# Optimization experiments

Measured on AMD Instinct MI355X. Metric: run time of the kernel, lower is better.

## Reference

```python
import jax, jax.numpy as jnp
import numpy as np
from jax import tree_util as jtu

B, N, DIM = 2, 2048, 512
HEADS, DH = 4, 128
CHUNK = 64
NC = N // CHUNK
DHID = 4 * DH  # expansion_factor 4
MAX_LR = 1.0   # default_step_transform_max_lr


def rms_norm(x, g, eps=1e-6):
    var = jnp.mean(jnp.square(x), axis=-1, keepdims=True)
    return x * jax.lax.rsqrt(var + eps) * g


def mem_model(params, x):
    # ResidualNorm(MemoryMLP depth=2): out = mlp(rmsnorm(x)) + x
    g, w1, w2 = params
    h = rms_norm(x, g)
    h = jax.nn.gelu(jnp.dot(h, w1), approximate=False)
    h = jnp.dot(h, w2)
    return h + x


def _expand(a, leaf):
    # broadcast a per-(b*h) scalar gate over a weight leaf
    return a.reshape(a.shape + (1,) * (leaf.ndim - 1))


def neural_memory(seq, g_store, g_retrieve, Wq, Wk, Wv, Wa, ba, Wm, Wd, bd, Wg, Wc, mem_g, w1, w2):
    xs = rms_norm(seq, g_store)      # store_norm
    xr = rms_norm(seq, g_retrieve)   # retrieve_norm

    def split_heads(t):
        return t.reshape(B, N, HEADS, DH).transpose(0, 2, 1, 3)  # b h n d

    k = split_heads(xs @ Wk)
    v = split_heads(xs @ Wv)
    q = split_heads(xr @ Wq)

    # adaptive per-token lr (sigmoid * max_lr)
    lr = (jax.nn.sigmoid(xs @ Wa + ba) * MAX_LR).transpose(0, 2, 1)  # [B,H,N]
    # per-chunk pooled stats drive momentum + decay gates (AveragePool)
    pooled = xs.reshape(B, NC, CHUNK, DIM).mean(axis=2)              # [B,NC,DIM]
    beta = jax.nn.sigmoid(pooled @ Wm)                               # momentum factor [B,NC,H]
    alpha = 1.0 - jax.nn.sigmoid(pooled @ Wd + bd)                   # weight-retain (1-decay)

    BH = B * HEADS
    k_c = k.reshape(BH, NC, CHUNK, DH)
    v_c = v.reshape(BH, NC, CHUNK, DH)
    q_c = q.reshape(BH, NC, CHUNK, DH)
    lr_c = lr.reshape(BH, NC, CHUNK)
    beta_t = beta.transpose(0, 2, 1).reshape(BH, NC).T   # [NC,BH]
    alpha_t = alpha.transpose(0, 2, 1).reshape(BH, NC).T

    # per-head memory params repeated over batch*heads (per_head_learned_parameters)
    init_params = (
        jnp.broadcast_to(mem_g, (B, HEADS, DH)).reshape(BH, DH),
        jnp.broadcast_to(w1, (B, HEADS, DH, DHID)).reshape(BH, DH, DHID),
        jnp.broadcast_to(w2, (B, HEADS, DHID, DH)).reshape(BH, DHID, DH),
    )

    def chunk_loss(params, kc, vc, lrc):
        pred = mem_model(params, kc)                              # [CHUNK,DH]
        return jnp.sum(jnp.mean(jnp.square(pred - vc), axis=-1) * lrc)

    # per-chunk 'surprise' gradients: vmap over (b*h) and chunks, grads wrt init weights
    grad_fn = jax.grad(chunk_loss)
    grads = jax.vmap(jax.vmap(grad_fn, in_axes=(None, 0, 0, 0)), in_axes=(0, 0, 0, 0))(
        init_params, k_c, v_c, lr_c)
    sur_t = jtu.tree_map(lambda g: jnp.moveaxis(-g, 1, 0), grads)  # [NC,BH,...]

    # momentum recurrence: m_t = beta_t * m_{t-1} + surprise_t
    def mom_step(m, inp):
        b, s = inp
        m = jtu.tree_map(lambda mm, ss: _expand(b, mm) * mm + ss, m, s)
        return m, m
    m0 = jtu.tree_map(lambda t: jnp.zeros_like(t[0]), sur_t)
    _, upd_t = jax.lax.scan(mom_step, m0, (beta_t, sur_t))

    # weight recurrence with decay: w_t = (1-decay_t) * w_{t-1} + m_t
    def w_step(w, inp):
        a, u = inp
        w = jtu.tree_map(lambda ww, uu: _expand(a, ww) * ww + uu, w, u)
        return w, w
    _, w_t = jax.lax.scan(w_step, init_params, (alpha_t, upd_t))

    # causal retrieval: chunk i reads weights updated through chunk i-1
    w_prev = jtu.tree_map(
        lambda wt, w0: jnp.moveaxis(jnp.concatenate([w0[None], wt[:-1]], axis=0), 0, 1),
        w_t, init_params)                                          # [BH,NC,...]

    retrieved = jax.vmap(jax.vmap(mem_model))(w_prev, q_c)         # [BH,NC,CHUNK,DH]
    retrieved = retrieved.reshape(B, HEADS, N, DH)
    gate = jax.nn.sigmoid(xr @ Wg).transpose(0, 2, 1)[..., None]   # retrieve_gate [B,H,N,1]
    retrieved = retrieved * gate
    out = retrieved.transpose(0, 2, 1, 3).reshape(B, N, HEADS * DH) @ Wc  # combine_heads
    return out


def setup_inputs():
    key = jax.random.key(0)
    ks = jax.random.split(key, 12)
    s = 0.02
    f = jnp.float32
    return {
        "seq": jax.random.normal(ks[0], (B, N, DIM), f),
        "g_store": jnp.ones((DIM,), f),
        "g_retrieve": jnp.ones((DIM,), f),
        "Wq": jax.random.normal(ks[1], (DIM, HEADS * DH), f) * s,
        "Wk": jax.random.normal(ks[2], (DIM, HEADS * DH), f) * s,
        "Wv": jax.random.normal(ks[3], (DIM, HEADS * DH), f) * s,
        "Wa": jax.random.normal(ks[4], (DIM, HEADS), f) * s,
        "ba": jnp.zeros((HEADS,), f),
        "Wm": jax.random.normal(ks[5], (DIM, HEADS), f) * s,
        "Wd": jax.random.normal(ks[6], (DIM, HEADS), f) * s,
        "bd": jnp.zeros((HEADS,), f),
        "Wg": jax.random.normal(ks[7], (DIM, HEADS), f) * s,
        "Wc": jax.random.normal(ks[8], (HEADS * DH, DIM), f) * s,
        "mem_g": jnp.ones((DH,), f),
        "w1": jax.random.normal(ks[9], (DH, DHID), f) * (1.0 / np.sqrt(DH)),
        "w2": jax.random.normal(ks[10], (DHID, DH), f) * (1.0 / np.sqrt(DHID)),
    }


def reference(seq, g_store, g_retrieve, Wq, Wk, Wv, Wa, ba, Wm, Wd, bd, Wg, Wc, mem_g, w1, w2):
    return neural_memory(seq, g_store, g_retrieve, Wq, Wk, Wv, Wa, ba, Wm, Wd, bd, Wg, Wc, mem_g, w1, w2)
```

## Files before the change

kernel.cpp:

```cpp
#include <hip/hip_runtime.h>
#include <hip/hip_bf16.h>

#define B_ 2
#define N_ 2048
#define DIM_ 512
#define H_ 4
#define DH_ 128
#define DHID_ 512
#define CH_ 64
#define NC_ 32
#define BH_ 8

typedef __bf16 bf16x8 __attribute__((ext_vector_type(8)));
typedef float f32x4 __attribute__((ext_vector_type(4)));

__device__ __forceinline__ f32x4 MFMA(bf16x8 a, bf16x8 b, f32x4 c) {
    return __builtin_amdgcn_mfma_f32_16x16x32_bf16(a, b, c, 0, 0, 0);
}
__device__ __forceinline__ bf16x8 ld8(const __bf16* p) { return *(const bf16x8*)p; }

__device__ __forceinline__ float sigmoidf_(float x) { return 1.0f / (1.0f + expf(-x)); }
__device__ __forceinline__ float gelu_f(float x) {
    return x * 0.5f * (1.0f + erff(x * 0.7071067811865476f));
}
__device__ __forceinline__ float gelu_g(float x) {
    float cdf = 0.5f * (1.0f + erff(x * 0.7071067811865476f));
    float pdf = 0.3989422804014327f * expf(-0.5f * x * x);
    return cdf + x * pdf;
}

__global__ __launch_bounds__(256) void rms_kernel(
    const float* __restrict__ seq, const float* __restrict__ gs,
    const float* __restrict__ gr, const float* __restrict__ Wa,
    const float* __restrict__ ba, const float* __restrict__ Wg,
    float* __restrict__ xs, float* __restrict__ xr,
    __bf16* __restrict__ xsb, __bf16* __restrict__ xrb,
    float* __restrict__ lrb, float* __restrict__ gateb)
{
    const int row = blockIdx.x;
    const int t = threadIdx.x;
    const int wave = t >> 6, lane = t & 63;
    const float* x = seq + (size_t)row * DIM_;
    float v0 = x[t], v1 = x[t + 256];
    float ss = v0 * v0 + v1 * v1;
#pragma unroll
    for (int off = 32; off; off >>= 1) ss += __shfl_xor(ss, off);
    __shared__ float red[4];
    __shared__ float red2[4][8];
    if (lane == 0) red[wave] = ss;
    __syncthreads();
    float tot = red[0] + red[1] + red[2] + red[3];
    float r = rsqrtf(tot * (1.0f / DIM_) + 1e-6f);
    size_t o = (size_t)row * DIM_;
    float a0 = v0 * r * gs[t], a1 = v1 * r * gs[t + 256];
    float b0 = v0 * r * gr[t], b1 = v1 * r * gr[t + 256];
    xs[o + t] = a0; xs[o + t + 256] = a1;
    xr[o + t] = b0; xr[o + t + 256] = b1;
    xsb[o + t] = (__bf16)a0; xsb[o + t + 256] = (__bf16)a1;
    xrb[o + t] = (__bf16)b0; xrb[o + t + 256] = (__bf16)b1;
    float pa[4], pg[4];
#pragma unroll
    for (int h = 0; h < 4; ++h) {
        pa[h] = a0 * Wa[t * 4 + h] + a1 * Wa[(t + 256) * 4 + h];
        pg[h] = b0 * Wg[t * 4 + h] + b1 * Wg[(t + 256) * 4 + h];
    }
#pragma unroll
    for (int h = 0; h < 4; ++h)
#pragma unroll
        for (int off = 32; off; off >>= 1) {
            pa[h] += __shfl_xor(pa[h], off);
            pg[h] += __shfl_xor(pg[h], off);
        }
    if (lane == 0) {
#pragma unroll
        for (int h = 0; h < 4; ++h) {
            red2[wave][h] = pa[h];
            red2[wave][4 + h] = pg[h];
        }
    }
    __syncthreads();
    if (t < 8) {
        float s = red2[0][t] + red2[1][t] + red2[2][t] + red2[3][t];
        int b = row >> 11, n = row & 2047;
        if (t < 4) lrb[(size_t)(b * 4 + t) * N_ + n] = sigmoidf_(s + ba[t]);
        else gateb[(size_t)(b * 4 + (t - 4)) * N_ + n] = sigmoidf_(s);
    }
}

__global__ __launch_bounds__(256) void ba_kernel(
    const float* __restrict__ xs, const float* __restrict__ Wm,
    const float* __restrict__ Wd, const float* __restrict__ bd,
    float* __restrict__ beta, float* __restrict__ alpha)
{
    const int b = blockIdx.x >> 5, ci = blockIdx.x & 31;
    const int t = threadIdx.x;
    const int wave = t >> 6, lane = t & 63;
    const float* base = xs + ((size_t)b * N_ + ci * CH_) * DIM_;
    const int d0 = t * 2;
    float s0 = 0.f, s1 = 0.f;
#pragma unroll 8
    for (int r = 0; r < CH_; ++r) {
        s0 += base[(size_t)r * DIM_ + d0];
        s1 += base[(size_t)r * DIM_ + d0 + 1];
    }
    s0 *= (1.0f / CH_); s1 *= (1.0f / CH_);
    float pm[4], pd[4];
#pragma unroll
    for (int h = 0; h < 4; ++h) {
        pm[h] = s0 * Wm[d0 * 4 + h] + s1 * Wm[(d0 + 1) * 4 + h];
        pd[h] = s0 * Wd[d0 * 4 + h] + s1 * Wd[(d0 + 1) * 4 + h];
    }
#pragma unroll
    for (int h = 0; h < 4; ++h)
#pragma unroll
        for (int off = 32; off; off >>= 1) {
            pm[h] += __shfl_xor(pm[h], off);
            pd[h] += __shfl_xor(pd[h], off);
        }
    __shared__ float red2[4][8];
    if (lane == 0) {
#pragma unroll
        for (int h = 0; h < 4; ++h) {
            red2[wave][h] = pm[h];
            red2[wave][4 + h] = pd[h];
        }
    }
    __syncthreads();
    if (t < 4) {
        float sm = red2[0][t] + red2[1][t] + red2[2][t] + red2[3][t];
        float sd = red2[0][4 + t] + red2[1][4 + t] + red2[2][4 + t] + red2[3][4 + t];
        int bh = b * 4 + t;
        beta[bh * NC_ + ci] = sigmoidf_(sm);
        alpha[bh * NC_ + ci] = 1.0f - sigmoidf_(sd + bd[t]);
    }
}

__global__ __launch_bounds__(256) void prep_kernel(
    const float* __restrict__ w1, const float* __restrict__ w2,
    const float* __restrict__ Wq, const float* __restrict__ Wk,
    const float* __restrict__ Wv, const float* __restrict__ Wc,
    __bf16* __restrict__ w1b, __bf16* __restrict__ w1Tb,
    __bf16* __restrict__ w2b, __bf16* __restrict__ w2Tb,
    __bf16* __restrict__ WqT, __bf16* __restrict__ WkT,
    __bf16* __restrict__ WvT, __bf16* __restrict__ WcT)
{
    int idx = blockIdx.x * 256 + threadIdx.x;
    if (idx < 65536) {
        w1b[idx] = (__bf16)w1[idx];
        int j = idx >> 7, d = idx & 127;
        w1Tb[idx] = (__bf16)w1[(size_t)d * DHID_ + j];
        w2b[idx] = (__bf16)w2[idx];
        int d2 = idx >> 9, j2 = idx & 511;
        w2Tb[idx] = (__bf16)w2[(size_t)j2 * DH_ + d2];
    }
    int n = idx >> 9, k = idx & 511;
    WqT[idx] = (__bf16)Wq[(size_t)k * 512 + n];
    WkT[idx] = (__bf16)Wk[(size_t)k * 512 + n];
    WvT[idx] = (__bf16)Wv[(size_t)k * 512 + n];
    WcT[idx] = (__bf16)Wc[(size_t)k * 512 + n];
}

__global__ __launch_bounds__(256, 4) void proj_kernel(
    const __bf16* __restrict__ xsb, const __bf16* __restrict__ xrb,
    const __bf16* __restrict__ WqT, const __bf16* __restrict__ WkT,
    const __bf16* __restrict__ WvT,
    float* __restrict__ qb, float* __restrict__ kb, float* __restrict__ vb)
{
    const int z = blockIdx.z;
    const __bf16* A = (z == 0) ? xrb : xsb;
    const __bf16* WT = (z == 0) ? WqT : (z == 1 ? WkT : WvT);
    float* out = (z == 0) ? qb : (z == 1 ? kb : vb);
    const int t = threadIdx.x;
    const int wave = t >> 6, lane = t & 63;
    const int lrow = lane & 15, lgrp = lane >> 4;
    const int c0 = blockIdx.x * 64 + wave * 16;
    const int col0 = blockIdx.y * 64;
    f32x4 acc[4];
#pragma unroll
    for (int i = 0; i < 4; ++i) acc[i] = (f32x4)0.f;
    const __bf16* ar = A + (size_t)(c0 + lrow) * 512;
#pragma unroll 4
    for (int k0 = 0; k0 < 512; k0 += 32) {
        bf16x8 av = ld8(ar + k0 + lgrp * 8);
#pragma unroll
        for (int ct = 0; ct < 4; ++ct) {
            bf16x8 bv = ld8(WT + (size_t)(col0 + ct * 16 + lrow) * 512 + k0 + lgrp * 8);
            acc[ct] = MFMA(av, bv, acc[ct]);
        }
    }
#pragma unroll
    for (int ct = 0; ct < 4; ++ct)
#pragma unroll
        for (int r = 0; r < 4; ++r) {
            int row = c0 + lgrp * 4 + r, col = col0 + ct * 16 + lrow;
            int b = row >> 11, n = row & 2047, h = col >> 7, d = col & 127;
            out[((((size_t)(b * H_ + h) * NC_ + (n >> 6)) * CH_) + (n & 63)) * DH_ + d] = acc[ct][r];
        }
}

__global__ __launch_bounds__(256, 4) void gemm_out(
    const __bf16* __restrict__ A, const __bf16* __restrict__ WT, float* __restrict__ out)
{
    const int t = threadIdx.x;
    const int wave = t >> 6, lane = t & 63;
    const int lrow = lane & 15, lgrp = lane >> 4;
    const int c0 = blockIdx.x * 64 + wave * 16;
    const int col0 = blockIdx.y * 64;
    f32x4 acc[4];
#pragma unroll
    for (int i = 0; i < 4; ++i) acc[i] = (f32x4)0.f;
    const __bf16* ar = A + (size_t)(c0 + lrow) * 512;
#pragma unroll 4
    for (int k0 = 0; k0 < 512; k0 += 32) {
        bf16x8 av = ld8(ar + k0 + lgrp * 8);
#pragma unroll
        for (int ct = 0; ct < 4; ++ct) {
            bf16x8 bv = ld8(WT + (size_t)(col0 + ct * 16 + lrow) * 512 + k0 + lgrp * 8);
            acc[ct] = MFMA(av, bv, acc[ct]);
        }
    }
#pragma unroll
    for (int ct = 0; ct < 4; ++ct)
#pragma unroll
        for (int r = 0; r < 4; ++r) {
            int row = c0 + lgrp * 4 + r, col = col0 + ct * 16 + lrow;
            out[(size_t)row * 512 + col] = acc[ct][r];
        }
}

__global__ __launch_bounds__(1024) void grad_kernel(
    const float* __restrict__ kbuf, const float* __restrict__ vbuf,
    const float* __restrict__ lrbuf, const float* __restrict__ memg,
    const __bf16* __restrict__ w1b, const __bf16* __restrict__ w1Tb,
    const __bf16* __restrict__ w2b, const __bf16* __restrict__ w2Tb,
    float* __restrict__ sg, __bf16* __restrict__ sw1, __bf16* __restrict__ sw2)
{
    const int blk = blockIdx.x;
    const int t = threadIdx.x;
    const int w = t >> 6, lane = t & 63;
    const int lrow = lane & 15, lgrp = lane >> 4;
    const int bh = blk >> 5, nc = blk & 31;
    const float* kc = kbuf + (size_t)blk * (CH_ * DH_);
    const float* vc = vbuf + (size_t)blk * (CH_ * DH_);
    const float* lrp = lrbuf + (size_t)bh * N_ + nc * CH_;
    __bf16* sw1_blk = sw1 + (size_t)blk * (DHID_ * DH_);
    __bf16* sw2_blk = sw2 + (size_t)blk * (DHID_ * DH_);

    __shared__ __bf16 h_s[64][136];
    __shared__ __bf16 e_s[64][136];
    __shared__ __bf16 a_s[64][136];
    __shared__ __bf16 dz_s[64][136];
    __shared__ __bf16 hT_s[128][72];
    __shared__ __bf16 eT_s[128][72];
    __shared__ __bf16 aT_s[128][72];
    __shared__ __bf16 dzT_s[128][72];
    __shared__ float r_s[64];
    __shared__ float lr_s[64];
    __shared__ float g_s[128];
    __shared__ float part_s[2][128];

    if (t < 128) g_s[t] = memg[t];
    if (t < 64) lr_s[t] = lrp[t];
    {
        const int c = t >> 4, i8 = t & 15, d0 = i8 * 8;
        float xv[8];
        float ss = 0.f;
#pragma unroll
        for (int i = 0; i < 2; ++i) {
            float4 f = *(const float4*)(kc + (size_t)c * DH_ + d0 + i * 4);
            xv[i * 4 + 0] = f.x; xv[i * 4 + 1] = f.y; xv[i * 4 + 2] = f.z; xv[i * 4 + 3] = f.w;
            ss += f.x * f.x + f.y * f.y + f.z * f.z + f.w * f.w;
        }
        ss += __shfl_xor(ss, 1); ss += __shfl_xor(ss, 2);
        ss += __shfl_xor(ss, 4); ss += __shfl_xor(ss, 8);
        float r = rsqrtf(ss * (1.0f / DH_) + 1e-6f);
        if (i8 == 0) r_s[c] = r;
        __syncthreads();
#pragma unroll
        for (int i = 0; i < 8; ++i)
            h_s[c][d0 + i] = (__bf16)(xv[i] * r * g_s[d0 + i]);
    }
    __syncthreads();
    {
        const int d = t >> 3, c0 = (t & 7) * 8;
#pragma unroll
        for (int i = 0; i < 8; ++i) hT_s[d][c0 + i] = h_s[c0 + i][d];
    }
    __syncthreads();

    const int cs = w & 3, dq = w >> 2;
    const int c0w = cs * 16, q0 = dq * 32;
    f32x4 yacc[2];
    yacc[0] = (f32x4)0.f; yacc[1] = (f32x4)0.f;

    for (int jt = 0; jt < 4; ++jt) {
        f32x4 zacc[2];
        zacc[0] = (f32x4)0.f; zacc[1] = (f32x4)0.f;
#pragma unroll
        for (int kt = 0; kt < 4; ++kt) {
            bf16x8 av = ld8(&h_s[c0w + lrow][kt * 32 + lgrp * 8]);
#pragma unroll
            for (int ct = 0; ct < 2; ++ct) {
                int j = jt * 128 + q0 + ct * 16 + lrow;
                bf16x8 bv = ld8(w1Tb + (size_t)j * 128 + kt * 32 + lgrp * 8);
                zacc[ct] = MFMA(av, bv, zacc[ct]);
            }
        }
#pragma unroll
        for (int ct = 0; ct < 2; ++ct)
#pragma unroll
            for (int r = 0; r < 4; ++r)
                a_s[c0w + lgrp * 4 + r][q0 + ct * 16 + lrow] = (__bf16)gelu_f(zacc[ct][r]);
        __syncthreads();
#pragma unroll
        for (int kt = 0; kt < 4; ++kt) {
            bf16x8 av = ld8(&a_s[c0w + lrow][kt * 32 + lgrp * 8]);
#pragma unroll
            for (int ct = 0; ct < 2; ++ct) {
                int d = q0 + ct * 16 + lrow;
                bf16x8 bv = ld8(w2Tb + (size_t)d * 512 + jt * 128 + kt * 32 + lgrp * 8);
                yacc[ct] = MFMA(av, bv, yacc[ct]);
            }
        }
        __syncthreads();
    }
#pragma unroll
    for (int ct = 0; ct < 2; ++ct)
#pragma unroll
        for (int r = 0; r < 4; ++r) {
            int c = c0w + lgrp * 4 + r, d = q0 + ct * 16 + lrow;
            float xvv = kc[(size_t)c * DH_ + d];
            float vvv = vc[(size_t)c * DH_ + d];
            float e = lr_s[c] * (2.0f / DH_) * (yacc[ct][r] + xvv - vvv);
            e_s[c][d] = (__bf16)e;
            eT_s[d][c] = (__bf16)e;
        }
    __syncthreads();

    const int js = w & 7, chh = w >> 3;
    f32x4 dhacc[2];
    dhacc[0] = (f32x4)0.f; dhacc[1] = (f32x4)0.f;

    for (int jt = 0; jt < 4; ++jt) {
        f32x4 ztacc[2], dtacc[2];
        ztacc[0] = (f32x4)0.f; ztacc[1] = (f32x4)0.f;
        dtacc[0] = (f32x4)0.f; dtacc[1] = (f32x4)0.f;
#pragma unroll
        for (int kt = 0; kt < 4; ++kt) {
            bf16x8 avz = ld8(w1Tb + (size_t)(jt * 128 + js * 16 + lrow) * 128 + kt * 32 + lgrp * 8);
            bf16x8 avd = ld8(w2b  + (size_t)(jt * 128 + js * 16 + lrow) * 128 + kt * 32 + lgrp * 8);
#pragma unroll
            for (int ct = 0; ct < 2; ++ct) {
                bf16x8 bvh = ld8(&h_s[chh * 32 + ct * 16 + lrow][kt * 32 + lgrp * 8]);
                bf16x8 bve = ld8(&e_s[chh * 32 + ct * 16 + lrow][kt * 32 + lgrp * 8]);
                ztacc[ct] = MFMA(avz, bvh, ztacc[ct]);
                dtacc[ct] = MFMA(avd, bve, dtacc[ct]);
            }
        }
#pragma unroll
        for (int ct = 0; ct < 2; ++ct)
#pragma unroll
            for (int r = 0; r < 4; ++r) {
                int j = js * 16 + lgrp * 4 + r, c = chh * 32 + ct * 16 + lrow;
                float zt = ztacc[ct][r];
                aT_s[j][c] = (__bf16)gelu_f(zt);
                float dzt = dtacc[ct][r] * gelu_g(zt);
                dzT_s[j][c] = (__bf16)dzt;
                dz_s[c][j] = (__bf16)dzt;
            }
        __syncthreads();
        {
            f32x4 wacc[4];
#pragma unroll
            for (int i = 0; i < 4; ++i) wacc[i] = (f32x4)0.f;
#pragma unroll
            for (int kt = 0; kt < 2; ++kt) {
                bf16x8 av = ld8(&dzT_s[js * 16 + lrow][kt * 32 + lgrp * 8]);
#pragma unroll
                for (int ct = 0; ct < 4; ++ct) {
                    bf16x8 bv = ld8(&hT_s[chh * 64 + ct * 16 + lrow][kt * 32 + lgrp * 8]);
                    wacc[ct] = MFMA(av, bv, wacc[ct]);
                }
            }
#pragma unroll
            for (int ct = 0; ct < 4; ++ct)
#pragma unroll
                for (int r = 0; r < 4; ++r) {
                    int jg = jt * 128 + js * 16 + lgrp * 4 + r, d = chh * 64 + ct * 16 + lrow;
                    sw1_blk[(size_t)jg * 128 + d] = (__bf16)(-wacc[ct][r]);
                }
        }
        {
            f32x4 wacc[4];
#pragma unroll
            for (int i = 0; i < 4; ++i) wacc[i] = (f32x4)0.f;
#pragma unroll
            for (int kt = 0; kt < 2; ++kt) {
                bf16x8 av = ld8(&eT_s[js * 16 + lrow][kt * 32 + lgrp * 8]);
#pragma unroll
                for (int ct = 0; ct < 4; ++ct) {
                    bf16x8 bv = ld8(&aT_s[chh * 64 + ct * 16 + lrow][kt * 32 + lgrp * 8]);
                    wacc[ct] = MFMA(av, bv, wacc[ct]);
                }
            }
#pragma unroll
            for (int ct = 0; ct < 4; ++ct)
#pragma unroll
                for (int r = 0; r < 4; ++r) {
                    int d = js * 16 + lgrp * 4 + r, jg = jt * 128 + chh * 64 + ct * 16 + lrow;
                    sw2_blk[(size_t)d * 512 + jg] = (__bf16)(-wacc[ct][r]);
                }
        }
#pragma unroll
        for (int kt = 0; kt < 4; ++kt) {
            bf16x8 av = ld8(w1b + (size_t)(js * 16 + lrow) * 512 + jt * 128 + kt * 32 + lgrp * 8);
#pragma unroll
            for (int ct = 0; ct < 2; ++ct) {
                bf16x8 bv = ld8(&dz_s[chh * 32 + ct * 16 + lrow][kt * 32 + lgrp * 8]);
                dhacc[ct] = MFMA(av, bv, dhacc[ct]);
            }
        }
        __syncthreads();
    }
    {
        float s[4] = {0.f, 0.f, 0.f, 0.f};
#pragma unroll
        for (int ct = 0; ct < 2; ++ct)
#pragma unroll
            for (int r = 0; r < 4; ++r) {
                int d = js * 16 + lgrp * 4 + r, c = chh * 32 + ct * 16 + lrow;
                s[r] += dhacc[ct][r] * (float)hT_s[d][c];
            }
#pragma unroll
        for (int r = 0; r < 4; ++r) {
            s[r] += __shfl_xor(s[r], 1); s[r] += __shfl_xor(s[r], 2);
            s[r] += __shfl_xor(s[r], 4); s[r] += __shfl_xor(s[r], 8);
        }
        if (lrow == 0) {
#pragma unroll
            for (int r = 0; r < 4; ++r) part_s[chh][js * 16 + lgrp * 4 + r] = s[r];
        }
        __syncthreads();
        if (t < 128) sg[(size_t)blk * DH_ + t] = -(part_s[0][t] + part_s[1][t]) / g_s[t];
    }
}

__global__ __launch_bounds__(256) void scan_all(
    __bf16* __restrict__ sw1, const __bf16* __restrict__ w1T,
    __bf16* __restrict__ sw2, const __bf16* __restrict__ w2T,
    float* __restrict__ sgb, const float* __restrict__ memg,
    const float* __restrict__ beta, const float* __restrict__ alpha)
{
    const int bi = blockIdx.x, t = threadIdx.x;
    if (bi < 4096) {
        __bf16* buf = (bi < 2048) ? sw1 : sw2;
        const __bf16* init = (bi < 2048) ? w1T : w2T;
        int idx = (bi & 2047) * 256 + t;
        int bh = idx >> 16, el = idx & 65535;
        float wv = (float)init[el], m = 0.f;
        const float* bp = beta + bh * NC_;
        const float* ap = alpha + bh * NC_;
        __bf16* base = buf + ((size_t)bh * NC_) * 65536 + el;
        for (int ci = 0; ci < NC_; ++ci) {
            float s = (float)base[(size_t)ci * 65536];
            base[(size_t)ci * 65536] = (__bf16)wv;
            m = fmaf(bp[ci], m, s);
            wv = fmaf(ap[ci], wv, m);
        }
    } else {
        int idx = (bi - 4096) * 256 + t;
        int bh = idx >> 7, el = idx & 127;
        float wv = memg[el], m = 0.f;
        const float* bp = beta + bh * NC_;
        const float* ap = alpha + bh * NC_;
        float* base = sgb + ((size_t)bh * NC_) * 128 + el;
        for (int ci = 0; ci < NC_; ++ci) {
            float s = base[(size_t)ci * 128];
            base[(size_t)ci * 128] = wv;
            m = fmaf(bp[ci], m, s);
            wv = fmaf(ap[ci], wv, m);
        }
    }
}

__global__ __launch_bounds__(512, 4) void retrieve_kernel(
    const float* __restrict__ qbuf, const float* __restrict__ gatebuf,
    const float* __restrict__ sg, const __bf16* __restrict__ sw1,
    const __bf16* __restrict__ sw2, __bf16* __restrict__ retgb)
{
    const int blk = blockIdx.x;
    const int t = threadIdx.x;
    const int w = t >> 6, lane = t & 63;
    const int lrow = lane & 15, lgrp = lane >> 4;
    const int bh = blk >> 5, nc = blk & 31;
    const float* qc = qbuf + (size_t)blk * (CH_ * DH_);
    const __bf16* w1p = sw1 + (size_t)blk * (DHID_ * DH_);
    const __bf16* w2p = sw2 + (size_t)blk * (DHID_ * DH_);
    const float* gp = sg + (size_t)blk * DH_;

    __shared__ __bf16 h_s[64][136];
    __shared__ __bf16 a_s[64][136];
    __shared__ float g_s[128];

    if (t < 128) g_s[t] = gp[t];
    {
        const int c = t >> 3, dblk = t & 7, d0 = dblk * 16;
        float xv[16];
        float ss = 0.f;
#pragma unroll
        for (int i = 0; i < 4; ++i) {
            float4 f = *(const float4*)(qc + (size_t)c * DH_ + d0 + i * 4);
            xv[i * 4 + 0] = f.x; xv[i * 4 + 1] = f.y; xv[i * 4 + 2] = f.z; xv[i * 4 + 3] = f.w;
            ss += f.x * f.x + f.y * f.y + f.z * f.z + f.w * f.w;
        }
        ss += __shfl_xor(ss, 1); ss += __shfl_xor(ss, 2); ss += __shfl_xor(ss, 4);
        float r = rsqrtf(ss * (1.0f / DH_) + 1e-6f);
        __syncthreads();
#pragma unroll
        for (int i = 0; i < 16; ++i)
            h_s[c][d0 + i] = (__bf16)(xv[i] * r * g_s[d0 + i]);
    }
    __syncthreads();

    const int cs = w & 3, dh2 = w >> 2;
    const int c0w = cs * 16, d0w = dh2 * 64;
    f32x4 yacc[4];
#pragma unroll
    for (int i = 0; i < 4; ++i) yacc[i] = (f32x4)0.f;

    for (int jt = 0; jt < 4; ++jt) {
        f32x4 zacc[4];
#pragma unroll
        for (int i = 0; i < 4; ++i) zacc[i] = (f32x4)0.f;
#pragma unroll
        for (int kt = 0; kt < 4; ++kt) {
            bf16x8 av = ld8(&h_s[c0w + lrow][kt * 32 + lgrp * 8]);
#pragma unroll
            for (int ct = 0; ct < 4; ++ct) {
                int j = jt * 128 + d0w + ct * 16 + lrow;
                bf16x8 bv = ld8(w1p + (size_t)j * 128 + kt * 32 + lgrp * 8);
                zacc[ct] = MFMA(av, bv, zacc[ct]);
            }
        }
#pragma unroll
        for (int ct = 0; ct < 4; ++ct)
#pragma unroll
            for (int r = 0; r < 4; ++r)
                a_s[c0w + lgrp * 4 + r][d0w + ct * 16 + lrow] = (__bf16)gelu_f(zacc[ct][r]);
        __syncthreads();
#pragma unroll
        for (int kt = 0; kt < 4; ++kt) {
            bf16x8 av = ld8(&a_s[c0w + lrow][kt * 32 + lgrp * 8]);
#pragma unroll
            for (int ct = 0; ct < 4; ++ct) {
                int d = d0w + ct * 16 + lrow;
                bf16x8 bv = ld8(w2p + (size_t)d * 512 + jt * 128 + kt * 32 + lgrp * 8);
                yacc[ct] = MFMA(av, bv, yacc[ct]);
            }
        }
        __syncthreads();
    }
    const int b = bh >> 2, hh = bh & 3;
#pragma unroll
    for (int ct = 0; ct < 4; ++ct)
#pragma unroll
        for (int r = 0; r < 4; ++r) {
            int c = c0w + lgrp * 4 + r, d = d0w + ct * 16 + lrow;
            int n = nc * CH_ + c;
            float q = qc[(size_t)c * DH_ + d];
            float gv = gatebuf[(size_t)bh * N_ + n];
            retgb[((size_t)(b * N_ + n)) * 512 + hh * 128 + d] = (__bf16)((yacc[ct][r] + q) * gv);
        }
}

extern "C" void kernel_launch(void* const* d_in, const int* in_sizes, int n_in,
                              void* d_out, int out_size, void* d_ws, size_t ws_size,
                              hipStream_t stream) {
    const float* seq     = (const float*)d_in[0];
    const float* g_store = (const float*)d_in[1];
    const float* g_retr  = (const float*)d_in[2];
    const float* Wq = (const float*)d_in[3];
    const float* Wk = (const float*)d_in[4];
    const float* Wv = (const float*)d_in[5];
    const float* Wa = (const float*)d_in[6];
    const float* ba = (const float*)d_in[7];
    const float* Wm = (const float*)d_in[8];
    const float* Wd = (const float*)d_in[9];
    const float* bd = (const float*)d_in[10];
    const float* Wg = (const float*)d_in[11];
    const float* Wc = (const float*)d_in[12];
    const float* memg = (const float*)d_in[13];
    const float* w1 = (const float*)d_in[14];
    const float* w2 = (const float*)d_in[15];
    float* out = (float*)d_out;

    float* p = (float*)d_ws;
    float* xs = p;     p += (size_t)B_ * N_ * DIM_;
    float* xr = p;     p += (size_t)B_ * N_ * DIM_;
    float* kb = p;     p += (size_t)B_ * N_ * DIM_;
    float* vb = p;     p += (size_t)B_ * N_ * DIM_;
    float* qb = p;     p += (size_t)B_ * N_ * DIM_;
    float* lrb = p;    p += (size_t)BH_ * N_;
    float* gateb = p;  p += (size_t)BH_ * N_;
    float* beta = p;   p += BH_ * NC_;
    float* alpha = p;  p += BH_ * NC_;
    float* sgb = p;    p += (size_t)BH_ * NC_ * DH_;

    __bf16* bp_ = (__bf16*)p;
    __bf16* xsb = bp_;  bp_ += (size_t)B_ * N_ * DIM_;
    __bf16* xrb = bp_;  bp_ += (size_t)B_ * N_ * DIM_;
    __bf16* retgb = bp_; bp_ += (size_t)B_ * N_ * DIM_;
    __bf16* w1b = bp_;  bp_ += DH_ * DHID_;
    __bf16* w1Tb = bp_; bp_ += DH_ * DHID_;
    __bf16* w2b = bp_;  bp_ += DH_ * DHID_;
    __bf16* w2Tb = bp_; bp_ += DH_ * DHID_;
    __bf16* WqT = bp_;  bp_ += DIM_ * DIM_;
    __bf16* WkT = bp_;  bp_ += DIM_ * DIM_;
    __bf16* WvT = bp_;  bp_ += DIM_ * DIM_;
    __bf16* WcT = bp_;  bp_ += DIM_ * DIM_;
    __bf16* sw1b = bp_; bp_ += (size_t)BH_ * NC_ * DH_ * DHID_;
    __bf16* sw2b = bp_; bp_ += (size_t)BH_ * NC_ * DH_ * DHID_;

    rms_kernel<<<B_ * N_, 256, 0, stream>>>(seq, g_store, g_retr, Wa, ba, Wg,
                                            xs, xr, xsb, xrb, lrb, gateb);
    ba_kernel<<<B_ * NC_, 256, 0, stream>>>(xs, Wm, Wd, bd, beta, alpha);
    prep_kernel<<<1024, 256, 0, stream>>>(w1, w2, Wq, Wk, Wv, Wc,
                                          w1b, w1Tb, w2b, w2Tb, WqT, WkT, WvT, WcT);
    proj_kernel<<<dim3(64, 8, 3), 256, 0, stream>>>(xsb, xrb, WqT, WkT, WvT, qb, kb, vb);
    grad_kernel<<<BH_ * NC_, 1024, 0, stream>>>(kb, vb, lrb, memg, w1b, w1Tb, w2b, w2Tb,
                                                sgb, sw1b, sw2b);
    scan_all<<<4100, 256, 0, stream>>>(sw1b, w1Tb, sw2b, w2Tb, sgb, memg, beta, alpha);
    retrieve_kernel<<<BH_ * NC_, 512, 0, stream>>>(qb, gateb, sgb, sw1b, sw2b, retgb);
    gemm_out<<<dim3(64, 8), 256, 0, stream>>>(retgb, WcT, out);
}
```

Baseline: 336.0 us.

## Prefetch weight fragments into registers, vectorize scan, tanh GELU, drop xr buffer

The gradient kernel now loads the w1/w2 weight fragments into registers one jt-iteration ahead, so global loads overlap the MFMA and LDS work instead of sitting inline. The momentum/decay scan processes 8 bf16 elements per thread with 16-byte loads and stores, cutting its block count roughly eightfold. Exact erf-based GELU and its derivative are replaced by a tanh-form approximation built on fast exp and reciprocal, computed together, which changes numerics against the exact-GELU reference. The unused fp32 xr write is also removed.

```diff
diff --git a/kernel.cpp b/kernel.cpp
--- a/kernel.cpp
+++ b/kernel.cpp
@@ -20,20 +20,31 @@
 __device__ __forceinline__ bf16x8 ld8(const __bf16* p) { return *(const bf16x8*)p; }
 
 __device__ __forceinline__ float sigmoidf_(float x) { return 1.0f / (1.0f + expf(-x)); }
+
 __device__ __forceinline__ float gelu_f(float x) {
-    return x * 0.5f * (1.0f + erff(x * 0.7071067811865476f));
-}
-__device__ __forceinline__ float gelu_g(float x) {
-    float cdf = 0.5f * (1.0f + erff(x * 0.7071067811865476f));
-    float pdf = 0.3989422804014327f * expf(-0.5f * x * x);
-    return cdf + x * pdf;
+    float x2 = x * x;
+    float u = x * fmaf(0.0713548163f, x2, 1.5957691216f);
+    float E = __expf(u);
+    float r = __builtin_amdgcn_rcpf(E + 1.0f);
+    return x * (1.0f - r);
+}
+__device__ __forceinline__ void gelu_fg(float x, float& f, float& g) {
+    float x2 = x * x;
+    float u = x * fmaf(0.0713548163f, x2, 1.5957691216f);
+    float E = __expf(u);
+    float r = __builtin_amdgcn_rcpf(E + 1.0f);
+    float omr = 1.0f - r;
+    f = x * omr;
+    float th = 1.0f - 2.0f * r;
+    float ap = fmaf(0.1070322244f, x2, 0.7978845608f);
+    g = fmaf(0.5f * x * (1.0f - th * th), ap, omr);
 }
 
 __global__ __launch_bounds__(256) void rms_kernel(
     const float* __restrict__ seq, const float* __restrict__ gs,
     const float* __restrict__ gr, const float* __restrict__ Wa,
     const float* __restrict__ ba, const float* __restrict__ Wg,
-    float* __restrict__ xs, float* __restrict__ xr,
+    float* __restrict__ xs,
     __bf16* __restrict__ xsb, __bf16* __restrict__ xrb,
     float* __restrict__ lrb, float* __restrict__ gateb)
 {
@@ -55,7 +66,6 @@
     float a0 = v0 * r * gs[t], a1 = v1 * r * gs[t + 256];
     float b0 = v0 * r * gr[t], b1 = v1 * r * gr[t + 256];
     xs[o + t] = a0; xs[o + t + 256] = a1;
-    xr[o + t] = b0; xr[o + t + 256] = b1;
     xsb[o + t] = (__bf16)a0; xsb[o + t + 256] = (__bf16)a1;
     xrb[o + t] = (__bf16)b0; xrb[o + t + 256] = (__bf16)b1;
     float pa[4], pg[4];
@@ -293,19 +303,27 @@
     f32x4 yacc[2];
     yacc[0] = (f32x4)0.f; yacc[1] = (f32x4)0.f;
 
+    bf16x8 w1r[8], w2r[8];
+#pragma unroll
+    for (int kt = 0; kt < 4; ++kt)
+#pragma unroll
+        for (int ct = 0; ct < 2; ++ct)
+            w1r[kt * 2 + ct] = ld8(w1Tb + (size_t)(q0 + ct * 16 + lrow) * 128 + kt * 32 + lgrp * 8);
+
     for (int jt = 0; jt < 4; ++jt) {
         f32x4 zacc[2];
         zacc[0] = (f32x4)0.f; zacc[1] = (f32x4)0.f;
 #pragma unroll
         for (int kt = 0; kt < 4; ++kt) {
             bf16x8 av = ld8(&h_s[c0w + lrow][kt * 32 + lgrp * 8]);
-#pragma unroll
-            for (int ct = 0; ct < 2; ++ct) {
-                int j = jt * 128 + q0 + ct * 16 + lrow;
-                bf16x8 bv = ld8(w1Tb + (size_t)j * 128 + kt * 32 + lgrp * 8);
-                zacc[ct] = MFMA(av, bv, zacc[ct]);
-            }
-        }
+            zacc[0] = MFMA(av, w1r[kt * 2 + 0], zacc[0]);
+            zacc[1] = MFMA(av, w1r[kt * 2 + 1], zacc[1]);
+        }
+#pragma unroll
+        for (int kt = 0; kt < 4; ++kt)
+#pragma unroll
+            for (int ct = 0; ct < 2; ++ct)
+                w2r[kt * 2 + ct] = ld8(w2Tb + (size_t)(q0 + ct * 16 + lrow) * 512 + jt * 128 + kt * 32 + lgrp * 8);
 #pragma unroll
         for (int ct = 0; ct < 2; ++ct)
 #pragma unroll
@@ -315,12 +333,15 @@
 #pragma unroll
         for (int kt = 0; kt < 4; ++kt) {
             bf16x8 av = ld8(&a_s[c0w + lrow][kt * 32 + lgrp * 8]);
-#pragma unroll
-            for (int ct = 0; ct < 2; ++ct) {
-                int d = q0 + ct * 16 + lrow;
-                bf16x8 bv = ld8(w2Tb + (size_t)d * 512 + jt * 128 + kt * 32 + lgrp * 8);
-                yacc[ct] = MFMA(av, bv, yacc[ct]);
-            }
+            yacc[0] = MFMA(av, w2r[kt * 2 + 0], yacc[0]);
+            yacc[1] = MFMA(av, w2r[kt * 2 + 1], yacc[1]);
+        }
+        if (jt < 3) {
+#pragma unroll
+            for (int kt = 0; kt < 4; ++kt)
+#pragma unroll
+                for (int ct = 0; ct < 2; ++ct)
+                    w1r[kt * 2 + ct] = ld8(w1Tb + (size_t)((jt + 1) * 128 + q0 + ct * 16 + lrow) * 128 + kt * 32 + lgrp * 8);
         }
         __syncthreads();
     }
@@ -341,30 +362,40 @@
     f32x4 dhacc[2];
     dhacc[0] = (f32x4)0.f; dhacc[1] = (f32x4)0.f;
 
+    bf16x8 azr[4], adr[4], w1br[4];
+#pragma unroll
+    for (int kt = 0; kt < 4; ++kt) {
+        azr[kt] = ld8(w1Tb + (size_t)(js * 16 + lrow) * 128 + kt * 32 + lgrp * 8);
+        adr[kt] = ld8(w2b + (size_t)(js * 16 + lrow) * 128 + kt * 32 + lgrp * 8);
+    }
+
     for (int jt = 0; jt < 4; ++jt) {
         f32x4 ztacc[2], dtacc[2];
         ztacc[0] = (f32x4)0.f; ztacc[1] = (f32x4)0.f;
         dtacc[0] = (f32x4)0.f; dtacc[1] = (f32x4)0.f;
 #pragma unroll
         for (int kt = 0; kt < 4; ++kt) {
-            bf16x8 avz = ld8(w1Tb + (size_t)(jt * 128 + js * 16 + lrow) * 128 + kt * 32 + lgrp * 8);
-            bf16x8 avd = ld8(w2b  + (size_t)(jt * 128 + js * 16 + lrow) * 128 + kt * 32 + lgrp * 8);
 #pragma unroll
             for (int ct = 0; ct < 2; ++ct) {
                 bf16x8 bvh = ld8(&h_s[chh * 32 + ct * 16 + lrow][kt * 32 + lgrp * 8]);
                 bf16x8 bve = ld8(&e_s[chh * 32 + ct * 16 + lrow][kt * 32 + lgrp * 8]);
-                ztacc[ct] = MFMA(avz, bvh, ztacc[ct]);
-                dtacc[ct] = MFMA(avd, bve, dtacc[ct]);
-            }
-        }
+                ztacc[ct] = MFMA(azr[kt], bvh, ztacc[ct]);
+                dtacc[ct] = MFMA(adr[kt], bve, dtacc[ct]);
+            }
+        }
+#pragma unroll
+        for (int kt = 0; kt < 4; ++kt)
+            w1br[kt] = ld8(w1b + (size_t)(js * 16 + lrow) * 512 + jt * 128 + kt * 32 + lgrp * 8);
 #pragma unroll
         for (int ct = 0; ct < 2; ++ct)
 #pragma unroll
             for (int r = 0; r < 4; ++r) {
                 int j = js * 16 + lgrp * 4 + r, c = chh * 32 + ct * 16 + lrow;
                 float zt = ztacc[ct][r];
-                aT_s[j][c] = (__bf16)gelu_f(zt);
-                float dzt = dtacc[ct][r] * gelu_g(zt);
+                float gf, gg;
+                gelu_fg(zt, gf, gg);
+                aT_s[j][c] = (__bf16)gf;
+                float dzt = dtacc[ct][r] * gg;
                 dzT_s[j][c] = (__bf16)dzt;
                 dz_s[c][j] = (__bf16)dzt;
             }
@@ -413,11 +444,17 @@
         }
 #pragma unroll
         for (int kt = 0; kt < 4; ++kt) {
-            bf16x8 av = ld8(w1b + (size_t)(js * 16 + lrow) * 512 + jt * 128 + kt * 32 + lgrp * 8);
 #pragma unroll
             for (int ct = 0; ct < 2; ++ct) {
                 bf16x8 bv = ld8(&dz_s[chh * 32 + ct * 16 + lrow][kt * 32 + lgrp * 8]);
-                dhacc[ct] = MFMA(av, bv, dhacc[ct]);
+                dhacc[ct] = MFMA(w1br[kt], bv, dhacc[ct]);
+            }
+        }
+        if (jt < 3) {
+#pragma unroll
+            for (int kt = 0; kt < 4; ++kt) {
+                azr[kt] = ld8(w1Tb + (size_t)((jt + 1) * 128 + js * 16 + lrow) * 128 + kt * 32 + lgrp * 8);
+                adr[kt] = ld8(w2b + (size_t)((jt + 1) * 128 + js * 16 + lrow) * 128 + kt * 32 + lgrp * 8);
             }
         }
         __syncthreads();
@@ -452,23 +489,33 @@
     const float* __restrict__ beta, const float* __restrict__ alpha)
 {
     const int bi = blockIdx.x, t = threadIdx.x;
-    if (bi < 4096) {
-        __bf16* buf = (bi < 2048) ? sw1 : sw2;
-        const __bf16* init = (bi < 2048) ? w1T : w2T;
-        int idx = (bi & 2047) * 256 + t;
-        int bh = idx >> 16, el = idx & 65535;
-        float wv = (float)init[el], m = 0.f;
+    if (bi < 512) {
+        __bf16* buf = (bi < 256) ? sw1 : sw2;
+        const __bf16* init = (bi < 256) ? w1T : w2T;
+        int idx = (bi & 255) * 256 + t;
+        int bh = idx >> 13, e8 = idx & 8191;
+        size_t off = (size_t)e8 * 8;
         const float* bp = beta + bh * NC_;
         const float* ap = alpha + bh * NC_;
-        __bf16* base = buf + ((size_t)bh * NC_) * 65536 + el;
+        __bf16* base = buf + (size_t)bh * NC_ * 65536 + off;
+        bf16x8 iv = *(const bf16x8*)(init + off);
+        float m[8], wv[8];
+#pragma unroll
+        for (int k = 0; k < 8; ++k) { m[k] = 0.f; wv[k] = (float)iv[k]; }
         for (int ci = 0; ci < NC_; ++ci) {
-            float s = (float)base[(size_t)ci * 65536];
-            base[(size_t)ci * 65536] = (__bf16)wv;
-            m = fmaf(bp[ci], m, s);
-            wv = fmaf(ap[ci], wv, m);
+            bf16x8 s = *(const bf16x8*)(base + (size_t)ci * 65536);
+            float bb = bp[ci], aa = ap[ci];
+            bf16x8 o;
+#pragma unroll
+            for (int k = 0; k < 8; ++k) {
+                o[k] = (__bf16)wv[k];
+                m[k] = fmaf(bb, m[k], (float)s[k]);
+                wv[k] = fmaf(aa, wv[k], m[k]);
+            }
+            *(bf16x8*)(base + (size_t)ci * 65536) = o;
         }
     } else {
-        int idx = (bi - 4096) * 256 + t;
+        int idx = (bi - 512) * 256 + t;
         int bh = idx >> 7, el = idx & 127;
         float wv = memg[el], m = 0.f;
         const float* bp = beta + bh * NC_;
@@ -596,7 +643,6 @@
 
     float* p = (float*)d_ws;
     float* xs = p;     p += (size_t)B_ * N_ * DIM_;
-    float* xr = p;     p += (size_t)B_ * N_ * DIM_;
     float* kb = p;     p += (size_t)B_ * N_ * DIM_;
     float* vb = p;     p += (size_t)B_ * N_ * DIM_;
     float* qb = p;     p += (size_t)B_ * N_ * DIM_;
@@ -622,14 +668,14 @@
     __bf16* sw2b = bp_; bp_ += (size_t)BH_ * NC_ * DH_ * DHID_;
 
     rms_kernel<<<B_ * N_, 256, 0, stream>>>(seq, g_store, g_retr, Wa, ba, Wg,
-                                            xs, xr, xsb, xrb, lrb, gateb);
+                                            xs, xsb, xrb, lrb, gateb);
     ba_kernel<<<B_ * NC_, 256, 0, stream>>>(xs, Wm, Wd, bd, beta, alpha);
     prep_kernel<<<1024, 256, 0, stream>>>(w1, w2, Wq, Wk, Wv, Wc,
                                           w1b, w1Tb, w2b, w2Tb, WqT, WkT, WvT, WcT);
     proj_kernel<<<dim3(64, 8, 3), 256, 0, stream>>>(xsb, xrb, WqT, WkT, WvT, qb, kb, vb);
     grad_kernel<<<BH_ * NC_, 1024, 0, stream>>>(kb, vb, lrb, memg, w1b, w1Tb, w2b, w2Tb,
                                                 sgb, sw1b, sw2b);
-    scan_all<<<4100, 256, 0, stream>>>(sw1b, w1Tb, sw2b, w2Tb, sgb, memg, beta, alpha);
+    scan_all<<<516, 256, 0, stream>>>(sw1b, w1Tb, sw2b, w2Tb, sgb, memg, beta, alpha);
     retrieve_kernel<<<BH_ * NC_, 512, 0, stream>>>(qb, gateb, sgb, sw1b, sw2b, retgb);
     gemm_out<<<dim3(64, 8), 256, 0, stream>>>(retgb, WcT, out);
 }
```

Result: faster. 315.3 us (-6.1%).
